# Performance work log

Hardware: AMD Instinct MI355X
Metric: run time of the kernel (lower is better)

Reference implementation:

```python
import jax, jax.numpy as jnp
import numpy as np

EPS = 1e-6
H = 16       # query heads
KVH = 8      # kv heads
DH = 64      # head dim
HID = 1024


def _rms_norm(x, w, eps=EPS):
    ms = jnp.mean(jnp.square(x.astype(jnp.float32)), axis=-1, keepdims=True) + eps
    y = x.astype(jnp.float32) * jax.lax.rsqrt(ms)
    if w is not None:
        y = y * w.astype(jnp.float32)
    return y.astype(x.dtype)


def _rotate_half(x):
    h = x.shape[-1] // 2
    return jnp.concatenate([-x[..., h:], x[..., :h]], axis=-1)


def _multi_axis_rope(x, cos, sin, ndim):
    # x: [B,S,Hd,DH]; cos/sin: [S, rot_total]
    dh = x.shape[-1]
    rot = 2 * (dh // (2 * ndim))
    outs = []
    for i in range(ndim):
        sl = slice(i * rot, (i + 1) * rot)
        xp = x[..., sl]
        cp = cos[:, sl][:, None, :]   # [S,1,rot] broadcasts over heads
        sp = sin[:, sl][:, None, :]
        outs.append(xp * cp + _rotate_half(xp) * sp)
    return jnp.concatenate(outs, axis=-1)


def setup_inputs() -> dict:
    key = jax.random.key(0)
    ks = jax.random.split(key, 10)
    B, S = 4, 2048
    inp = {
        "hidden_states": jax.random.normal(ks[0], (B, S, HID), dtype=jnp.float32),
        "cos": jax.random.uniform(ks[1], (S, DH), dtype=jnp.float32, minval=-1.0, maxval=1.0),
        "sin": jax.random.uniform(ks[2], (S, DH), dtype=jnp.float32, minval=-1.0, maxval=1.0),
        "position_ids": jax.random.randint(ks[3], (B, S, 2), 0, 64).astype(jnp.int64),
        "attention_mask": jnp.ones((B, S), dtype=bool),
        "Wq": jax.random.normal(ks[4], (HID, H * DH), dtype=jnp.float32) * 0.02,
        "Wk": jax.random.normal(ks[5], (HID, KVH * DH), dtype=jnp.float32) * 0.02,
        "Wv": jax.random.normal(ks[6], (HID, KVH * DH), dtype=jnp.float32) * 0.02,
        "Wo": jax.random.normal(ks[7], (H * DH, HID), dtype=jnp.float32) * 0.02,
        "q_norm_w": jnp.ones((DH,), dtype=jnp.float32),
        "k_norm_w": jnp.ones((DH,), dtype=jnp.float32),
    }
    return inp


def reference(hidden_states, cos, sin, position_ids, attention_mask, Wq, Wk, Wv, Wo, q_norm_w, k_norm_w):
    B, S, _ = hidden_states.shape
    ndim = int(position_ids.shape[-1])

    q = (hidden_states @ Wq).reshape(B, S, H, DH)
    k = (hidden_states @ Wk).reshape(B, S, KVH, DH)
    v = (hidden_states @ Wv).reshape(B, S, KVH, DH)

    q = _rms_norm(q, q_norm_w)
    k = _rms_norm(k, k_norm_w)
    v = _rms_norm(v, None)  # v_norm has no scale

    q = _multi_axis_rope(q, cos, sin, ndim)
    k = _multi_axis_rope(k, cos, sin, ndim)

    # [B, heads, S, DH]; repeat kv heads for GQA
    q = q.transpose(0, 2, 1, 3)
    k = jnp.repeat(k.transpose(0, 2, 1, 3), H // KVH, axis=1)
    v = jnp.repeat(v.transpose(0, 2, 1, 3), H // KVH, axis=1)

    scores = jnp.einsum("bhqd,bhkd->bhqk", q, k)  # scaling = 1.0
    key_mask = attention_mask[:, None, None, :]
    scores = jnp.where(key_mask, scores, jnp.finfo(scores.dtype).min)
    probs = jax.nn.softmax(scores.astype(jnp.float32), axis=-1).astype(v.dtype)

    out = jnp.einsum("bhqk,bhkd->bhqd", probs, v)
    out = out.transpose(0, 2, 1, 3).reshape(B, S, H * DH)
    out = jnp.where(attention_mask[:, :, None], out, 0.0)
    return out @ Wo
```

## Files before the change

### kernel.cpp

```cpp
#include <hip/hip_runtime.h>
#include <stdint.h>
#include <stddef.h>

typedef unsigned short u16;
typedef unsigned int   u32;
typedef unsigned short u16x8 __attribute__((ext_vector_type(8)));
typedef __attribute__((ext_vector_type(8))) __bf16 bf16x8;
typedef __attribute__((ext_vector_type(4))) float f32x4;

__device__ __forceinline__ float bf2f(u16 v){
  union { unsigned u; float f; } x; x.u = ((unsigned)v) << 16; return x.f;
}
__device__ __forceinline__ u16 f2bf(float f){
  union { float f; unsigned u; } x; x.f = f;
  return (u16)((x.u + 0x7fffu + ((x.u >> 16) & 1u)) >> 16);
}

__device__ __forceinline__ float exp2_fast(float x){
  float r; asm("v_exp_f32 %0, %1" : "=v"(r) : "v"(x)); return r;
}
__device__ __forceinline__ u32 cvt_pk_bf16(float lo, float hi){
  u32 r; asm("v_cvt_pk_bf16_f32 %0, %1, %2" : "=v"(r) : "v"(lo), "v"(hi)); return r;
}

__device__ __forceinline__ f32x4 mfma16(bf16x8 a, bf16x8 b, f32x4 c){
  return __builtin_amdgcn_mfma_f32_16x16x32_bf16(a, b, c, 0, 0, 0);
}

#define AS1 __attribute__((address_space(1)))
#define AS3 __attribute__((address_space(3)))
__device__ __forceinline__ void gload_lds16(const void* g, void* l){
  __builtin_amdgcn_global_load_lds((const AS1 void*)g, (AS3 void*)l, 16, 0, 0);
}

__global__ void f32_to_bf16_swz(const float* __restrict__ in, u16* __restrict__ out,
                                int total_chunks){
  for (int i = blockIdx.x * blockDim.x + threadIdx.x; i < total_chunks;
       i += gridDim.x * blockDim.x){
    int row = i >> 7, c = i & 127;
    int cs = (c & ~7) | ((c & 7) ^ (row & 7));
    const float* p = in + ((size_t)i << 3);
    float4 v0 = *(const float4*)p;
    float4 v1 = *(const float4*)(p + 4);
    u16x8 o = { f2bf(v0.x), f2bf(v0.y), f2bf(v0.z), f2bf(v0.w),
                f2bf(v1.x), f2bf(v1.y), f2bf(v1.z), f2bf(v1.w) };
    *(u16x8*)(out + (((size_t)row << 7) + cs) * 8) = o;
  }
}

__global__ void conv_transpose_swz(const float* __restrict__ in, u16* __restrict__ out,
                                   int R, int C){
  __shared__ float t[32][33];
  int c0 = blockIdx.x * 32, r0 = blockIdx.y * 32;
  int tx = threadIdx.x, ty = threadIdx.y;
  t[ty][tx] = in[(size_t)(r0 + ty) * C + c0 + tx];
  __syncthreads();
  int tid = ty * 32 + tx;
  if (tid < 128){
    int orow = tid >> 2, oc = tid & 3;
    int gr = c0 + orow;
    int gc = (r0 >> 3) + oc;
    int gcs = (gc & ~7) | ((gc & 7) ^ (gr & 7));
    u16x8 v;
#pragma unroll
    for (int i = 0; i < 8; i++) v[i] = f2bf(t[oc * 8 + i][orow]);
    *(u16x8*)(out + (size_t)gr * R + gcs * 8) = v;
  }
}

__global__ void pack_cs(const float* __restrict__ cosb, const float* __restrict__ sinb,
                        float2* __restrict__ cs, int n){
  int i = blockIdx.x * 256 + threadIdx.x;
  if (i < n) cs[i] = (float2){cosb[i], sinb[i]};
}

template<int BM, int WM, int EPI>
__global__ __launch_bounds__(512, 2)
void gemm256(const u16* __restrict__ A, const u16* __restrict__ Bt,
             void* __restrict__ Cv, int M, int N, int K,
             const float2* __restrict__ cs, const float* __restrict__ qw,
             const float* __restrict__ kw, u16* __restrict__ Qn,
             u16* __restrict__ Kn, u16* __restrict__ Vn){
  constexpr int MF = WM / 16;
  constexpr int ALOADS = BM / 64;
  __shared__ __align__(16) u16 Ab[3][BM * 64];
  const int tid = threadIdx.x;
  const int wid = tid >> 6, lane = tid & 63;
  const int g = lane >> 4, col = lane & 15;
  const int wm = wid >> 2, wn = wid & 3;
  const int swz = col & 7;

  int nb  = gridDim.x * gridDim.y;
  int lid = blockIdx.y * gridDim.x + blockIdx.x;
  int cpx = nb >> 3;
  int sid = (lid & 7) * cpx + (lid >> 3);
  int bx  = sid % gridDim.x, by = sid / gridDim.x;
  const int m0 = by * BM, n0 = bx * 256;

  f32x4 acc[MF][4];
#pragma unroll
  for (int i = 0; i < MF; i++)
#pragma unroll
    for (int j = 0; j < 4; j++) acc[i][j] = (f32x4){0.f, 0.f, 0.f, 0.f};

  const int arow = wid * 8 + (lane >> 3);
  const int acl  = (lane & 7) * 8;

  auto STAGE_A = [&](int bi, int k0){
#pragma unroll
    for (int j = 0; j < ALOADS; j++)
      gload_lds16(A + (size_t)(m0 + j * 64 + arow) * K + k0 + acl,
                  &Ab[bi][j * 4096 + wid * 512]);
  };

  const int NT = K >> 6;
  STAGE_A(0, 0);
  STAGE_A(1, 64);
  if (ALOADS == 4) asm volatile("s_waitcnt vmcnt(4)");
  else             asm volatile("s_waitcnt vmcnt(2)");
  __builtin_amdgcn_sched_barrier(0);
  __builtin_amdgcn_s_barrier();
  __builtin_amdgcn_sched_barrier(0);

  int cb = 0, sa = 2;
  for (int t = 0; t < NT; ++t){
    bf16x8 bfr[4][2];
#pragma unroll
    for (int ni = 0; ni < 4; ni++){
      const u16* bp = Bt + (size_t)(n0 + wn * 64 + ni * 16 + col) * K + t * 64;
#pragma unroll
      for (int ks = 0; ks < 2; ks++)
        bfr[ni][ks] = *(const bf16x8*)(bp + (((ks * 4 + g) ^ swz) << 3));
    }
    __builtin_amdgcn_sched_barrier(0);
    if (t + 2 < NT) STAGE_A(sa, (t + 2) * 64);
    __builtin_amdgcn_sched_barrier(0);

    const u16* Ac = &Ab[cb][0];
#pragma unroll
    for (int ph = 0; ph < MF / 4; ++ph){
      bf16x8 afr[4][2];
#pragma unroll
      for (int m2 = 0; m2 < 4; m2++){
        int row = wm * WM + (ph * 4 + m2) * 16 + col;
#pragma unroll
        for (int ks = 0; ks < 2; ks++)
          afr[m2][ks] = *(const bf16x8*)&Ac[row * 64 + (((ks * 4 + g) ^ swz) << 3)];
      }
      __builtin_amdgcn_s_setprio(1);
#pragma unroll
      for (int m2 = 0; m2 < 4; m2++)
#pragma unroll
        for (int ni = 0; ni < 4; ni++)
#pragma unroll
          for (int ks = 0; ks < 2; ks++)
            acc[ph * 4 + m2][ni] =
                mfma16(afr[m2][ks], bfr[ni][ks], acc[ph * 4 + m2][ni]);
      __builtin_amdgcn_s_setprio(0);
    }

    asm volatile("s_waitcnt lgkmcnt(0)");
    __builtin_amdgcn_sched_barrier(0);
    if (t + 2 < NT){
      if (ALOADS == 4) asm volatile("s_waitcnt vmcnt(4)");
      else             asm volatile("s_waitcnt vmcnt(2)");
    } else {
      asm volatile("s_waitcnt vmcnt(0)");
    }
    __builtin_amdgcn_sched_barrier(0);
    __builtin_amdgcn_s_barrier();
    __builtin_amdgcn_sched_barrier(0);
    cb = (cb == 2) ? 0 : cb + 1;
    sa = (sa == 2) ? 0 : sa + 1;
  }

  if (EPI == 1){
    const int colbase = n0 + wn * 64;
    const int t0 = m0 + wm * WM;
    const int bb = t0 >> 11;
    if (colbase < 1536){
      const bool isQ = colbase < 1024;
      const int head = isQ ? (colbase >> 6) : ((colbase - 1024) >> 6);
      const float* wp = isQ ? qw : kw;
      float wv[4];
#pragma unroll
      for (int ni = 0; ni < 4; ni++) wv[ni] = wp[ni * 16 + col];
      u16* outp = isQ ? Qn : Kn;
      size_t hb = isQ ? ((size_t)(bb * 16 + head) * 2048)
                      : ((size_t)(bb * 8 + head) * 2048);
#pragma unroll
      for (int mi = 0; mi < MF; mi++){
        f32x4 ssv = (f32x4){0.f, 0.f, 0.f, 0.f};
#pragma unroll
        for (int ni = 0; ni < 4; ni++)
#pragma unroll
          for (int r = 0; r < 4; r++) ssv[r] += acc[mi][ni][r] * acc[mi][ni][r];
#pragma unroll
        for (int off = 1; off < 16; off <<= 1)
#pragma unroll
          for (int r = 0; r < 4; r++) ssv[r] += __shfl_xor(ssv[r], off, 64);
        f32x4 rinv;
#pragma unroll
        for (int r = 0; r < 4; r++) rinv[r] = rsqrtf(ssv[r] * (1.f / 64.f) + 1e-6f);
        int s0 = (t0 + mi * 16 + g * 4) & 2047;
#pragma unroll
        for (int np = 0; np < 2; np++){
          int d0 = np * 32 + col, d1 = d0 + 16;
#pragma unroll
          for (int r = 0; r < 4; r++){
            int s = s0 + r;
            float y0 = acc[mi][np * 2][r]     * rinv[r] * wv[np * 2];
            float y1 = acc[mi][np * 2 + 1][r] * rinv[r] * wv[np * 2 + 1];
            float2 c0 = cs[s * 64 + d0];
            float2 c1 = cs[s * 64 + d1];
            float o0 = y0 * c0.x - y1 * c0.y;
            float o1 = y1 * c1.x + y0 * c1.y;
            if (isQ){
              outp[(hb + s) * 64 + d0] = f2bf(o0);
              outp[(hb + s) * 64 + d1] = f2bf(o1);
            } else {
              int z0 = ((((d0 >> 3) ^ s) & 7) << 3) | (d0 & 7);
              int z1 = ((((d1 >> 3) ^ s) & 7) << 3) | (d1 & 7);
              outp[(hb + s) * 64 + z0] = f2bf(o0);
              outp[(hb + s) * 64 + z1] = f2bf(o1);
            }
          }
        }
      }
    } else {
      const int kvh = (colbase - 1536) >> 6;
      const size_t vb0 = (size_t)(bb * 8 + kvh) * 64;
#pragma unroll
      for (int mi = 0; mi < MF; mi++){
        f32x4 ssv = (f32x4){0.f, 0.f, 0.f, 0.f};
#pragma unroll
        for (int ni = 0; ni < 4; ni++)
#pragma unroll
          for (int r = 0; r < 4; r++) ssv[r] += acc[mi][ni][r] * acc[mi][ni][r];
#pragma unroll
        for (int off = 1; off < 16; off <<= 1)
#pragma unroll
          for (int r = 0; r < 4; r++) ssv[r] += __shfl_xor(ssv[r], off, 64);
        f32x4 rinv;
#pragma unroll
        for (int r = 0; r < 4; r++) rinv[r] = rsqrtf(ssv[r] * (1.f / 64.f) + 1e-6f);
        int s0 = (t0 + mi * 16 + g * 4) & 2047;
#pragma unroll
        for (int ni = 0; ni < 4; ni++){
          int d = ni * 16 + col;
          uint2 o;
          o.x = cvt_pk_bf16(acc[mi][ni][0] * rinv[0], acc[mi][ni][1] * rinv[1]);
          o.y = cvt_pk_bf16(acc[mi][ni][2] * rinv[2], acc[mi][ni][3] * rinv[3]);
          size_t addr = (vb0 + d) * 2048 + (s0 & ~63)
                      + ((((s0 >> 3) ^ (d & 7)) & 7) << 3) + (s0 & 7);
          *(uint2*)(Vn + addr) = o;
        }
      }
    }
    return;
  }

#pragma unroll
  for (int mi = 0; mi < MF; mi++)
#pragma unroll
    for (int ni = 0; ni < 4; ni++)
#pragma unroll
      for (int r = 0; r < 4; r++){
        int row = m0 + wm * WM + mi * 16 + g * 4 + r;
        int cc  = n0 + wn * 64 + ni * 16 + col;
        ((float*)Cv)[(size_t)row * N + cc] = acc[mi][ni][r];
      }
}

__global__ __launch_bounds__(512, 2)
void flash_attn(const u16* __restrict__ Qn, const u16* __restrict__ Kn,
                const u16* __restrict__ Vn, u16* __restrict__ AO){
  const int S = 2048;
  const float L2E = 1.4426950408889634f;
  const float C2 = 30.f;
  const int b = blockIdx.z, h = blockIdx.y, qt = blockIdx.x;
  const int kvh = h >> 1;
  const int wid = threadIdx.x >> 6, lane = threadIdx.x & 63;
  const int kg = wid >> 2, wq = wid & 3;
  const int g = lane >> 4, col = lane & 15;
  const int q0 = qt * 256 + wq * 64;

  __shared__ __align__(16) u16 lds[40960];
  u16* Kl = lds + kg * 8192;
  u16* Vl = lds + 16384 + kg * 8192;
  char* Pw = (char*)(lds + 32768 + wid * 1024);

  bf16x8 ones;
#pragma unroll
  for (int i = 0; i < 8; i++) ones[i] = (__bf16)1.0f;

  bf16x8 aq[4][2];
#pragma unroll
  for (int cg = 0; cg < 4; cg++){
    const u16* qp = Qn + ((size_t)((b * 16 + h) * S) + q0 + cg * 16 + col) * 64;
    aq[cg][0] = *(const bf16x8*)(qp + g * 8);
    aq[cg][1] = *(const bf16x8*)(qp + 32 + g * 8);
  }

  const u16* Kbase = Kn + (size_t)(b * 8 + kvh) * S * 64 + (size_t)kg * 1024 * 64;
  const u16* Vbase = Vn + (size_t)(b * 8 + kvh) * 64 * S;
  const int vcol0 = kg * 1024;

  f32x4 acc[4][4];
  f32x4 lacc[4];
#pragma unroll
  for (int cg = 0; cg < 4; cg++){
    lacc[cg] = (f32x4){0.f, 0.f, 0.f, 0.f};
#pragma unroll
    for (int i = 0; i < 4; i++) acc[cg][i] = (f32x4){0.f, 0.f, 0.f, 0.f};
  }

  const int sw = col & 7;
  const int pswz = sw << 4;

  auto STAGE = [&](int bi, int ktl){
    int kc0 = ktl * 64;
#pragma unroll
    for (int cc = 0; cc < 2; cc++){
      int chunk = cc * 4 + wq;
      gload_lds16(Kbase + (size_t)kc0 * 64 + chunk * 512 + lane * 8,
                  Kl + bi * 4096 + chunk * 512);
      int drow = chunk * 8 + (lane >> 3);
      gload_lds16(Vbase + (size_t)drow * S + vcol0 + kc0 + (lane & 7) * 8,
                  Vl + bi * 4096 + chunk * 512);
    }
  };

  int buf = 0;
  STAGE(0, 0);
  __syncthreads();

  for (int kt = 0; kt < 16; ++kt){
    if (kt + 1 < 16) STAGE(buf ^ 1, kt + 1);

    const u16* Kb = Kl + buf * 4096;
    const u16* Vb = Vl + buf * 4096;

    bf16x8 kf[4][2], vf[4][2];
#pragma unroll
    for (int c = 0; c < 4; c++){
      const u16* kb = Kb + (c * 16 + col) * 64;
      kf[c][0] = *(const bf16x8*)(kb + (g ^ sw) * 8);
      kf[c][1] = *(const bf16x8*)(kb + ((4 + g) ^ sw) * 8);
      const u16* vb = Vb + (c * 16 + col) * 64;
      vf[c][0] = *(const bf16x8*)(vb + (g ^ sw) * 8);
      vf[c][1] = *(const bf16x8*)(vb + ((4 + g) ^ sw) * 8);
    }

#pragma unroll
    for (int cg = 0; cg < 4; cg++){
      f32x4 sf[4];
      __builtin_amdgcn_s_setprio(1);
#pragma unroll
      for (int c = 0; c < 4; c++){
        f32x4 z = (f32x4){0.f, 0.f, 0.f, 0.f};
        z = mfma16(kf[c][0], aq[cg][0], z);
        sf[c] = mfma16(kf[c][1], aq[cg][1], z);
      }
      __builtin_amdgcn_s_setprio(0);

#pragma unroll
      for (int c = 0; c < 4; c++){
        float p0 = exp2_fast(__builtin_fmaf(sf[c][0], L2E, -C2));
        float p1 = exp2_fast(__builtin_fmaf(sf[c][1], L2E, -C2));
        float p2 = exp2_fast(__builtin_fmaf(sf[c][2], L2E, -C2));
        float p3 = exp2_fast(__builtin_fmaf(sf[c][3], L2E, -C2));
        uint2 pw;
        pw.x = cvt_pk_bf16(p0, p1);
        pw.y = cvt_pk_bf16(p2, p3);
        *(uint2*)(Pw + ((col * 128 + c * 32 + g * 8) ^ pswz)) = pw;
      }

      bf16x8 pf0 = *(const bf16x8*)(Pw + ((col * 128 + g * 16) ^ pswz));
      bf16x8 pf1 = *(const bf16x8*)(Pw + ((col * 128 + 64 + g * 16) ^ pswz));
      __builtin_amdgcn_s_setprio(1);
#pragma unroll
      for (int cd = 0; cd < 4; cd++){
        acc[cg][cd] = mfma16(vf[cd][0], pf0, acc[cg][cd]);
        acc[cg][cd] = mfma16(vf[cd][1], pf1, acc[cg][cd]);
      }
      lacc[cg] = mfma16(ones, pf0, lacc[cg]);
      lacc[cg] = mfma16(ones, pf1, lacc[cg]);
      __builtin_amdgcn_s_setprio(0);
    }

    __syncthreads();
    buf ^= 1;
  }

  f32x4* sAcc = (f32x4*)lds;
  float*  sL  = (float*)(lds + 32768);
  if (kg == 1){
#pragma unroll
    for (int cg = 0; cg < 4; cg++){
#pragma unroll
      for (int cd = 0; cd < 4; cd++)
        sAcc[(cg * 4 + cd) * 256 + wq * 64 + lane] = acc[cg][cd];
      sL[cg * 256 + wq * 64 + lane] = lacc[cg][0];
    }
  }
  __syncthreads();
  if (kg == 0){
#pragma unroll
    for (int cg = 0; cg < 4; cg++){
      float l = lacc[cg][0] + sL[cg * 256 + wq * 64 + lane];
      float linv = 1.f / l;
      int s = q0 + cg * 16 + col;
#pragma unroll
      for (int cd = 0; cd < 4; cd++){
        f32x4 a = acc[cg][cd] + sAcc[(cg * 4 + cd) * 256 + wq * 64 + lane];
        uint2 o;
        o.x = cvt_pk_bf16(a[0] * linv, a[1] * linv);
        o.y = cvt_pk_bf16(a[2] * linv, a[3] * linv);
        int pc = (cd * 2 + (g >> 1)) ^ sw;
        *(uint2*)(AO + (size_t)(b * S + s) * 1024 + h * 64 + pc * 8 + (g & 1) * 4) = o;
      }
    }
  }
}

extern "C" void kernel_launch(void* const* d_in, const int* in_sizes, int n_in,
                              void* d_out, int out_size, void* d_ws, size_t ws_size,
                              hipStream_t stream){
  const int Btok = 8192;
  const float* hs   = (const float*)d_in[0];
  const float* cosb = (const float*)d_in[1];
  const float* sinb = (const float*)d_in[2];
  const float* Wq = (const float*)d_in[5];
  const float* Wk = (const float*)d_in[6];
  const float* Wv = (const float*)d_in[7];
  const float* Wo = (const float*)d_in[8];
  const float* qw = (const float*)d_in[9];
  const float* kw = (const float*)d_in[10];
  float* out = (float*)d_out;

  char* ws = (char*)d_ws;
  u16* hsB   = (u16*)ws;               ws += (size_t)Btok * 1024 * 2;
  u16* WqkvT = (u16*)ws;               ws += (size_t)2048 * 1024 * 2;
  u16* WoT   = (u16*)ws;               ws += (size_t)1024 * 1024 * 2;
  u16* Qn    = (u16*)ws;               ws += (size_t)Btok * 1024 * 2;
  u16* Kn    = (u16*)ws;               ws += (size_t)Btok * 512  * 2;
  u16* Vn    = (u16*)ws;               ws += (size_t)Btok * 512  * 2;
  float2* cst = (float2*)ws;           ws += (size_t)2048 * 64 * 8;
  u16* AO    = hsB;

  f32_to_bf16_swz<<<2048, 256, 0, stream>>>(hs, hsB, Btok * 128);

  dim3 tb(32, 32);
  conv_transpose_swz<<<dim3(32, 32), tb, 0, stream>>>(Wq, WqkvT,               1024, 1024);
  conv_transpose_swz<<<dim3(16, 32), tb, 0, stream>>>(Wk, WqkvT + 1024 * 1024, 1024, 512);
  conv_transpose_swz<<<dim3(16, 32), tb, 0, stream>>>(Wv, WqkvT + 1536 * 1024, 1024, 512);
  conv_transpose_swz<<<dim3(32, 32), tb, 0, stream>>>(Wo, WoT,                 1024, 1024);
  pack_cs<<<512, 256, 0, stream>>>(cosb, sinb, cst, 2048 * 64);

  gemm256<256, 128, 1><<<dim3(8, 32), 512, 0, stream>>>(
      hsB, WqkvT, nullptr, Btok, 2048, 1024, cst, qw, kw, Qn, Kn, Vn);

  flash_attn<<<dim3(8, 16, 4), 512, 0, stream>>>(Qn, Kn, Vn, AO);

  gemm256<128, 64, 2><<<dim3(4, 64), 512, 0, stream>>>(
      AO, WoT, out, Btok, 1024, 1024, nullptr, nullptr, nullptr,
      nullptr, nullptr, nullptr);
}
```

Measured before the change: 186.2 us.

## Feed P to PV MFMA from registers using 16x16x16 bf16 instructions

```diff
diff --git a/kernel.cpp b/kernel.cpp
--- a/kernel.cpp
+++ b/kernel.cpp
@@ -6,6 +6,8 @@
 typedef unsigned int   u32;
 typedef unsigned short u16x8 __attribute__((ext_vector_type(8)));
 typedef __attribute__((ext_vector_type(8))) __bf16 bf16x8;
+typedef __attribute__((ext_vector_type(4))) __bf16 bf16x4;
+typedef __attribute__((ext_vector_type(4))) short s16x4;
 typedef __attribute__((ext_vector_type(4))) float f32x4;
 
 __device__ __forceinline__ float bf2f(u16 v){
@@ -25,6 +27,11 @@
 
 __device__ __forceinline__ f32x4 mfma16(bf16x8 a, bf16x8 b, f32x4 c){
   return __builtin_amdgcn_mfma_f32_16x16x32_bf16(a, b, c, 0, 0, 0);
+}
+__device__ __forceinline__ f32x4 mfma16k(bf16x4 a, bf16x4 b, f32x4 c){
+  union { bf16x4 h; s16x4 s; } ua, ub;
+  ua.h = a; ub.h = b;
+  return __builtin_amdgcn_mfma_f32_16x16x16bf16_1k(ua.s, ub.s, c, 0, 0, 0);
 }
 
 #define AS1 __attribute__((address_space(1)))
@@ -285,14 +292,13 @@
   const int g = lane >> 4, col = lane & 15;
   const int q0 = qt * 256 + wq * 64;
 
-  __shared__ __align__(16) u16 lds[40960];
+  __shared__ __align__(16) u16 lds[34816];
   u16* Kl = lds + kg * 8192;
   u16* Vl = lds + 16384 + kg * 8192;
-  char* Pw = (char*)(lds + 32768 + wid * 1024);
-
-  bf16x8 ones;
-#pragma unroll
-  for (int i = 0; i < 8; i++) ones[i] = (__bf16)1.0f;
+
+  bf16x4 ones4;
+#pragma unroll
+  for (int i = 0; i < 4; i++) ones4[i] = (__bf16)1.0f;
 
   bf16x8 aq[4][2];
 #pragma unroll
@@ -316,7 +322,6 @@
   }
 
   const int sw = col & 7;
-  const int pswz = sw << 4;
 
   auto STAGE = [&](int bi, int ktl){
     int kc0 = ktl * 64;
@@ -341,15 +346,21 @@
     const u16* Kb = Kl + buf * 4096;
     const u16* Vb = Vl + buf * 4096;
 
-    bf16x8 kf[4][2], vf[4][2];
+    bf16x8 kf[4][2];
 #pragma unroll
     for (int c = 0; c < 4; c++){
       const u16* kb = Kb + (c * 16 + col) * 64;
       kf[c][0] = *(const bf16x8*)(kb + (g ^ sw) * 8);
       kf[c][1] = *(const bf16x8*)(kb + ((4 + g) ^ sw) * 8);
-      const u16* vb = Vb + (c * 16 + col) * 64;
-      vf[c][0] = *(const bf16x8*)(vb + (g ^ sw) * 8);
-      vf[c][1] = *(const bf16x8*)(vb + ((4 + g) ^ sw) * 8);
+    }
+    bf16x4 vf[4][4];
+#pragma unroll
+    for (int cd = 0; cd < 4; cd++){
+      const u16* vb = Vb + (cd * 16 + col) * 64;
+#pragma unroll
+      for (int c = 0; c < 4; c++)
+        vf[cd][c] = *(const bf16x4*)(vb + (((c * 2 + (g >> 1)) ^ sw) << 3)
+                                        + (g & 1) * 4);
     }
 
 #pragma unroll
@@ -364,28 +375,27 @@
       }
       __builtin_amdgcn_s_setprio(0);
 
+      bf16x4 pb[4];
 #pragma unroll
       for (int c = 0; c < 4; c++){
         float p0 = exp2_fast(__builtin_fmaf(sf[c][0], L2E, -C2));
         float p1 = exp2_fast(__builtin_fmaf(sf[c][1], L2E, -C2));
         float p2 = exp2_fast(__builtin_fmaf(sf[c][2], L2E, -C2));
         float p3 = exp2_fast(__builtin_fmaf(sf[c][3], L2E, -C2));
-        uint2 pw;
-        pw.x = cvt_pk_bf16(p0, p1);
-        pw.y = cvt_pk_bf16(p2, p3);
-        *(uint2*)(Pw + ((col * 128 + c * 32 + g * 8) ^ pswz)) = pw;
-      }
-
-      bf16x8 pf0 = *(const bf16x8*)(Pw + ((col * 128 + g * 16) ^ pswz));
-      bf16x8 pf1 = *(const bf16x8*)(Pw + ((col * 128 + 64 + g * 16) ^ pswz));
+        union { uint2 u; bf16x4 h; } pu;
+        pu.u.x = cvt_pk_bf16(p0, p1);
+        pu.u.y = cvt_pk_bf16(p2, p3);
+        pb[c] = pu.h;
+      }
+
       __builtin_amdgcn_s_setprio(1);
 #pragma unroll
-      for (int cd = 0; cd < 4; cd++){
-        acc[cg][cd] = mfma16(vf[cd][0], pf0, acc[cg][cd]);
-        acc[cg][cd] = mfma16(vf[cd][1], pf1, acc[cg][cd]);
-      }
-      lacc[cg] = mfma16(ones, pf0, lacc[cg]);
-      lacc[cg] = mfma16(ones, pf1, lacc[cg]);
+      for (int c = 0; c < 4; c++){
+        lacc[cg] = mfma16k(ones4, pb[c], lacc[cg]);
+#pragma unroll
+        for (int cd = 0; cd < 4; cd++)
+          acc[cg][cd] = mfma16k(vf[cd][c], pb[c], acc[cg][cd]);
+      }
       __builtin_amdgcn_s_setprio(0);
     }
 
@@ -394,7 +404,7 @@
   }
 
   f32x4* sAcc = (f32x4*)lds;
-  float*  sL  = (float*)(lds + 32768);
+  float*  sL  = (float*)((char*)lds + 65536);
   if (kg == 1){
 #pragma unroll
     for (int cg = 0; cg < 4; cg++){
```

Measured after the change: 200.3 us. 1.08x slower.
